# Optimization experiments

Measured on AMD Instinct MI355X. Metric: run time of the kernel, lower is better.

## Reference

```python
import jax, jax.numpy as jnp
import numpy as np

N_HEADS, N_KV_HEADS, HEAD_DIM = 32, 8, 128
N_REP = N_HEADS // N_KV_HEADS


def apply_rope(x, cos, sin):
    # x: [B, H, T, D]; cos/sin: [T, D/2]. Interleaved complex rotation (LLaMA style).
    x1 = x[..., 0::2]
    x2 = x[..., 1::2]
    c = cos[None, None, :, :]
    s = sin[None, None, :, :]
    r1 = x1 * c - x2 * s
    r2 = x1 * s + x2 * c
    return jnp.stack([r1, r2], axis=-1).reshape(x.shape)


def setup_inputs() -> dict:
    key = jax.random.key(0)
    ks = jax.random.split(key, 7)
    B, T, D = 1, 2048, 4096
    sc = 0.02
    return {
        "x": jax.random.normal(ks[0], (B, T, D), jnp.float32),
        "cos": jnp.cos(jax.random.normal(ks[1], (T, HEAD_DIM // 2), jnp.float32)),
        "sin": jnp.sin(jax.random.normal(ks[1], (T, HEAD_DIM // 2), jnp.float32)),
        "wq": jax.random.normal(ks[2], (D, D), jnp.float32) * sc,
        "wk": jax.random.normal(ks[3], (N_KV_HEADS * HEAD_DIM, D), jnp.float32) * sc,
        "wv": jax.random.normal(ks[4], (N_KV_HEADS * HEAD_DIM, D), jnp.float32) * sc,
        "wo": jax.random.normal(ks[5], (D, D), jnp.float32) * sc,
    }


def reference(x, cos, sin, wq, wk, wv, wo):
    B, T, _ = x.shape
    # QKV projections (nn.Linear: y = x @ W^T)
    q = (x @ wq.T).reshape(B, T, N_HEADS, HEAD_DIM).transpose(0, 2, 1, 3)
    k = (x @ wk.T).reshape(B, T, N_KV_HEADS, HEAD_DIM).transpose(0, 2, 1, 3)
    v = (x @ wv.T).reshape(B, T, N_KV_HEADS, HEAD_DIM).transpose(0, 2, 1, 3)
    # RoPE on q, k
    q = apply_rope(q, cos[:T], sin[:T])
    k = apply_rope(k, cos[:T], sin[:T])
    # GQA: repeat_interleave kv heads along head dim
    if N_REP > 1:
        k = jnp.repeat(k, N_REP, axis=1)
        v = jnp.repeat(v, N_REP, axis=1)
    # causal SDPA
    scale = 1.0 / jnp.sqrt(jnp.float32(HEAD_DIM))
    scores = jnp.einsum("bhqd,bhkd->bhqk", q, k) * scale
    causal = jnp.tril(jnp.ones((T, T), dtype=bool))
    scores = jnp.where(causal[None, None], scores, jnp.finfo(scores.dtype).min)
    attn = jax.nn.softmax(scores, axis=-1)
    y = jnp.einsum("bhqk,bhkd->bhqd", attn, v)
    y = y.transpose(0, 2, 1, 3).reshape(B, T, -1)
    return y @ wo.T
```

## Files before the change

### kernel.cpp

```cpp
#include <hip/hip_runtime.h>
#include <stdint.h>

typedef unsigned short ushort_t;
typedef __attribute__((ext_vector_type(8))) __bf16 bf16x8;
typedef __attribute__((ext_vector_type(4))) float f32x4;
typedef __attribute__((ext_vector_type(16))) float f32x16;

#define MFMA16(a, b, c) __builtin_amdgcn_mfma_f32_16x16x32_bf16((a), (b), (c), 0, 0, 0)
#define MFMA32(a, b, c) __builtin_amdgcn_mfma_f32_32x32x16_bf16((a), (b), (c), 0, 0, 0)

__device__ __forceinline__ ushort_t f2bf(float f) {
    unsigned u = __float_as_uint(f);
    u += 0x7fffu + ((u >> 16) & 1u);
    return (ushort_t)(u >> 16);
}

typedef __attribute__((address_space(1))) const unsigned char g_u8;
typedef __attribute__((address_space(3))) unsigned char l_u8;
__device__ __forceinline__ void gload16(const void* g, void* l) {
    __builtin_amdgcn_global_load_lds((g_u8*)g, (l_u8*)(unsigned int)(uintptr_t)l, 16, 0, 0);
}

__global__ __launch_bounds__(256) void cast_multi(const float* __restrict__ x,
                                                  const float* __restrict__ wq,
                                                  const float* __restrict__ wk,
                                                  const float* __restrict__ wv,
                                                  ushort_t* __restrict__ xb,
                                                  ushort_t* __restrict__ wqb,
                                                  ushort_t* __restrict__ wkb,
                                                  ushort_t* __restrict__ wvb) {
    int i = blockIdx.x * 256 + threadIdx.x;
    const float* in; ushort_t* out; int off;
    if (i < 2097152)      { in = x;  out = xb;  off = i; }
    else if (i < 6291456) { in = wq; out = wqb; off = i - 2097152; }
    else if (i < 7340032) { in = wk; out = wkb; off = i - 6291456; }
    else                  { in = wv; out = wvb; off = i - 7340032; }
    float4 v = ((const float4*)in)[off];
    ushort4 o;
    o.x = f2bf(v.x); o.y = f2bf(v.y); o.z = f2bf(v.z); o.w = f2bf(v.w);
    ((ushort4*)out)[off] = o;
}

__global__ __launch_bounds__(256) void cast_f32_bf16(const float* __restrict__ in,
                                                     ushort_t* __restrict__ out, int n4) {
    int i = blockIdx.x * 256 + threadIdx.x;
    if (i < n4) {
        float4 v = ((const float4*)in)[i];
        ushort4 o;
        o.x = f2bf(v.x); o.y = f2bf(v.y); o.z = f2bf(v.z); o.w = f2bf(v.w);
        ((ushort4*)out)[i] = o;
    }
}

#define GEMM_K_LOOP(Aarr, Barr, KDIM)                                                   \
    const ushort_t* aptr[4]; const ushort_t* bptr[4]; int ldsoff[4];                    \
    _Pragma("unroll")                                                                   \
    for (int p = 0; p < 4; p++) {                                                       \
        int s = p * 256 + tid;                                                          \
        int row = s >> 3;                                                               \
        int kc = (s & 7) ^ (row & 7);                                                   \
        aptr[p] = Aarr + (size_t)(bm + row) * (KDIM) + kc * 8;                          \
        bptr[p] = Barr + (size_t)(bn + row) * (KDIM) + kc * 8;                          \
        ldsoff[p] = s * 8;                                                              \
    }                                                                                   \
    const int l32 = lane & 31, hi = lane >> 5, r7 = l32 & 7;                            \
    for (int k0 = 0; k0 < (KDIM); k0 += 64) {                                           \
        _Pragma("unroll")                                                               \
        for (int p = 0; p < 4; p++) {                                                   \
            gload16(aptr[p] + k0, As + ldsoff[p]);                                      \
            gload16(bptr[p] + k0, Bs + ldsoff[p]);                                      \
        }                                                                               \
        __syncthreads();                                                                \
        _Pragma("unroll")                                                               \
        for (int ks = 0; ks < 4; ks++) {                                                \
            const int swz = ((ks * 2 + hi) ^ r7) << 3;                                  \
            bf16x8 a0 = *(const bf16x8*)(&As[(wm + l32) * 64 + swz]);                   \
            bf16x8 a1 = *(const bf16x8*)(&As[(wm + 32 + l32) * 64 + swz]);              \
            bf16x8 b0 = *(const bf16x8*)(&Bs[(wn + l32) * 64 + swz]);                   \
            bf16x8 b1 = *(const bf16x8*)(&Bs[(wn + 32 + l32) * 64 + swz]);              \
            acc[0][0] = MFMA32(a0, b0, acc[0][0]);                                      \
            acc[0][1] = MFMA32(a0, b1, acc[0][1]);                                      \
            acc[1][0] = MFMA32(a1, b0, acc[1][0]);                                      \
            acc[1][1] = MFMA32(a1, b1, acc[1][1]);                                      \
        }                                                                               \
        __syncthreads();                                                                \
    }

__global__ __launch_bounds__(256, 3) void gemm_qkv(const ushort_t* __restrict__ A,
                                                   const ushort_t* __restrict__ Wq,
                                                   const ushort_t* __restrict__ Wk,
                                                   const ushort_t* __restrict__ Wv,
                                                   ushort_t* __restrict__ Qo,
                                                   ushort_t* __restrict__ Ko,
                                                   ushort_t* __restrict__ VtO,
                                                   const float* __restrict__ cosp,
                                                   const float* __restrict__ sinp,
                                                   const float* __restrict__ wo,
                                                   ushort_t* __restrict__ wob) {
    const int by = blockIdx.y;
    const int tid = threadIdx.x;

    if (by >= 48) {
        const int ci = (by - 48) * gridDim.x + blockIdx.x;
        const float4* src = (const float4*)wo;
        ushort4* dst = (ushort4*)wob;
        int base = ci * 4096 + tid;
#pragma unroll
        for (int p = 0; p < 16; p++) {
            float4 v = src[base + p * 256];
            ushort4 o;
            o.x = f2bf(v.x); o.y = f2bf(v.y); o.z = f2bf(v.z); o.w = f2bf(v.w);
            dst[base + p * 256] = o;
        }
        return;
    }

    const ushort_t* B;
    int region, bn;
    if (by < 32)      { region = 0; B = Wq; bn = by * 128; }
    else if (by < 40) { region = 1; B = Wk; bn = (by - 32) * 128; }
    else              { region = 2; B = Wv; bn = (by - 40) * 128; }
    const int bm = blockIdx.x * 128;

    __shared__ __align__(16) ushort_t As[128 * 64];
    __shared__ __align__(16) ushort_t Bs[128 * 64];
    const int w = tid >> 6, lane = tid & 63;
    const int wm = (w >> 1) * 64, wn = (w & 1) * 64;
    f32x16 acc[2][2] = {};

    GEMM_K_LOOP(A, B, 4096)

    const float qscale = 0.08838834764831845f;
    if (region < 2) {
        ushort_t* C = (region == 0) ? Qo : Ko;
        const int Nc = (region == 0) ? 4096 : 1024;
        const float scl = (region == 0) ? qscale : 1.0f;
#pragma unroll
        for (int i = 0; i < 2; i++)
#pragma unroll
            for (int j = 0; j < 2; j++) {
                const int col = bn + wn + j * 32 + l32;
                const int pj = (col & 127) >> 1;
#pragma unroll
                for (int r = 0; r < 16; r++) {
                    const int row = bm + wm + i * 32 + (r & 3) + 8 * (r >> 2) + 4 * hi;
                    float v = acc[i][j][r];
                    float p = __shfl_xor(v, 1);
                    float c = cosp[row * 64 + pj], s = sinp[row * 64 + pj];
                    float res = (col & 1) ? fmaf(p, s, v * c)
                                          : (v * c - p * s);
                    C[(size_t)row * Nc + col] = f2bf(res * scl);
                }
            }
    } else {
#pragma unroll
        for (int i = 0; i < 2; i++)
#pragma unroll
            for (int j = 0; j < 2; j++) {
                const int col = bn + wn + j * 32 + l32;
#pragma unroll
                for (int g = 0; g < 4; g++) {
                    const int rowb = bm + wm + i * 32 + g * 8 + 4 * hi;
                    ushort4 pk;
                    pk.x = f2bf(acc[i][j][g * 4 + 0]);
                    pk.y = f2bf(acc[i][j][g * 4 + 1]);
                    pk.z = f2bf(acc[i][j][g * 4 + 2]);
                    pk.w = f2bf(acc[i][j][g * 4 + 3]);
                    *(ushort4*)(VtO + (size_t)col * 2048 + rowb) = pk;
                }
            }
    }
}

__global__ __launch_bounds__(256, 3) void gemm_bt(const ushort_t* __restrict__ A,
                                                  const ushort_t* __restrict__ B,
                                                  float* __restrict__ C,
                                                  int M, int N, int K) {
    const int bm = blockIdx.x * 128, bn = blockIdx.y * 128;
    __shared__ __align__(16) ushort_t As[128 * 64];
    __shared__ __align__(16) ushort_t Bs[128 * 64];
    const int tid = threadIdx.x;
    const int w = tid >> 6, lane = tid & 63;
    const int wm = (w >> 1) * 64, wn = (w & 1) * 64;
    f32x16 acc[2][2] = {};

    GEMM_K_LOOP(A, B, K)

#pragma unroll
    for (int i = 0; i < 2; i++)
#pragma unroll
        for (int j = 0; j < 2; j++) {
            const int col = bn + wn + j * 32 + l32;
#pragma unroll
            for (int r = 0; r < 16; r++) {
                const int row = bm + wm + i * 32 + (r & 3) + 8 * (r >> 2) + 4 * hi;
                C[(size_t)row * N + col] = acc[i][j][r];
            }
        }
}

__global__ __launch_bounds__(256) void flash_attn(const ushort_t* __restrict__ Q,
                                                  const ushort_t* __restrict__ Kp,
                                                  const ushort_t* __restrict__ Vt,
                                                  ushort_t* __restrict__ Y) {
    const int h = blockIdx.y, kh = h >> 2;
    const int tid = threadIdx.x;
    const int w = tid >> 6, lane = tid & 63;
    const int quad = lane >> 4, l16 = lane & 15;

    __shared__ __align__(16) ushort_t Ks[64 * 136];
    __shared__ __align__(16) ushort_t VtS[128 * 88];
    __shared__ __align__(16) ushort_t Ps[4 * 16 * 88];

    bf16x8 ones;
#pragma unroll
    for (int e = 0; e < 8; e++) ((ushort_t*)&ones)[e] = 0x3F80;

#pragma unroll 1
    for (int phase = 0; phase < 2; phase++) {
        const int qt = (phase == 0) ? blockIdx.x : 31 - blockIdx.x;

        bf16x8 qf[4];
        {
            const ushort_t* qrow = Q + (size_t)(qt * 64 + w * 16 + l16) * 4096 + h * 128 + quad * 8;
#pragma unroll
            for (int ks = 0; ks < 4; ks++) qf[ks] = *(const bf16x8*)(qrow + ks * 32);
        }

        f32x4 o[8] = {};
        f32x4 lacc = {};
        float m_i[4];
#pragma unroll
        for (int r = 0; r < 4; r++) m_i[r] = -1e30f;

        const int ntiles = qt + 1;
        for (int j = 0; j < ntiles; j++) {
            const int t0 = j * 64;
            {
#pragma unroll
                for (int p = 0; p < 4; p++) {
                    int ck = p * 256 + tid;
                    int r = ck >> 4, c = (ck & 15) * 8;
                    uint4 d = *(const uint4*)(Kp + (size_t)(t0 + r) * 1024 + kh * 128 + c);
                    *(uint4*)(&Ks[r * 136 + c]) = d;
                }
            }
            {
#pragma unroll
                for (int p = 0; p < 4; p++) {
                    int ck = p * 256 + tid;
                    int d = ck >> 3, c = (ck & 7) * 8;
                    uint4 v = *(const uint4*)(Vt + (size_t)(kh * 128 + d) * 2048 + t0 + c);
                    *(uint4*)(&VtS[d * 88 + c]) = v;
                }
            }
            __syncthreads();

            f32x4 s[4] = {};
#pragma unroll
            for (int ct = 0; ct < 4; ct++)
#pragma unroll
                for (int ks = 0; ks < 4; ks++) {
                    bf16x8 kf = *(const bf16x8*)(&Ks[(ct * 16 + l16) * 136 + ks * 32 + quad * 8]);
                    s[ct] = MFMA16(qf[ks], kf, s[ct]);
                }

            if (j == qt) {
#pragma unroll
                for (int ct = 0; ct < 4; ct++)
#pragma unroll
                    for (int r = 0; r < 4; r++) {
                        int rg = w * 16 + quad * 4 + r;
                        int cg = ct * 16 + l16;
                        if (cg > rg) s[ct][r] = -1e30f;
                    }
            }

            float alpha[4];
#pragma unroll
            for (int r = 0; r < 4; r++) {
                float v = fmaxf(fmaxf(s[0][r], s[1][r]), fmaxf(s[2][r], s[3][r]));
                v = fmaxf(v, __shfl_xor(v, 1));
                v = fmaxf(v, __shfl_xor(v, 2));
                v = fmaxf(v, __shfl_xor(v, 4));
                v = fmaxf(v, __shfl_xor(v, 8));
                float mn = fmaxf(m_i[r], v);
                alpha[r] = __expf(m_i[r] - mn);
                m_i[r] = mn;
            }
#pragma unroll
            for (int ct = 0; ct < 4; ct++)
#pragma unroll
                for (int r = 0; r < 4; r++)
                    s[ct][r] = __expf(s[ct][r] - m_i[r]);
#pragma unroll
            for (int n = 0; n < 8; n++)
#pragma unroll
                for (int r = 0; r < 4; r++) o[n][r] *= alpha[r];
#pragma unroll
            for (int r = 0; r < 4; r++) lacc[r] *= alpha[r];

#pragma unroll
            for (int ct = 0; ct < 4; ct++)
#pragma unroll
                for (int r = 0; r < 4; r++)
                    Ps[w * 1408 + (quad * 4 + r) * 88 + ct * 16 + l16] = f2bf(s[ct][r]);
            __threadfence_block();

#pragma unroll
            for (int ks2 = 0; ks2 < 2; ks2++) {
                bf16x8 pf = *(const bf16x8*)(&Ps[w * 1408 + l16 * 88 + ks2 * 32 + quad * 8]);
                lacc = MFMA16(pf, ones, lacc);
#pragma unroll
                for (int n = 0; n < 8; n++) {
                    bf16x8 vf = *(const bf16x8*)(&VtS[(n * 16 + l16) * 88 + ks2 * 32 + quad * 8]);
                    o[n] = MFMA16(pf, vf, o[n]);
                }
            }
            __syncthreads();
        }

        float inv[4];
#pragma unroll
        for (int r = 0; r < 4; r++) inv[r] = 1.0f / lacc[r];
#pragma unroll
        for (int n = 0; n < 8; n++)
#pragma unroll
            for (int r = 0; r < 4; r++) {
                int row = qt * 64 + w * 16 + quad * 4 + r;
                int col = h * 128 + n * 16 + l16;
                Y[(size_t)row * 4096 + col] = f2bf(o[n][r] * inv[r]);
            }
    }
}

extern "C" void kernel_launch(void* const* d_in, const int* in_sizes, int n_in,
                              void* d_out, int out_size, void* d_ws, size_t ws_size,
                              hipStream_t stream) {
    const float* x    = (const float*)d_in[0];
    const float* cosp = (const float*)d_in[1];
    const float* sinp = (const float*)d_in[2];
    const float* wq   = (const float*)d_in[3];
    const float* wk   = (const float*)d_in[4];
    const float* wv   = (const float*)d_in[5];
    const float* wo   = (const float*)d_in[6];
    float* out = (float*)d_out;

    ushort_t* xb   = (ushort_t*)d_ws;
    ushort_t* qb   = xb  + (size_t)2048 * 4096;
    ushort_t* yb   = qb  + (size_t)2048 * 4096;
    ushort_t* kb   = yb  + (size_t)2048 * 4096;
    ushort_t* vtb  = kb  + (size_t)2048 * 1024;
    ushort_t* wkb  = vtb + (size_t)1024 * 2048;
    ushort_t* wvb  = wkb + (size_t)1024 * 4096;
    ushort_t* wbig = wvb + (size_t)1024 * 4096;
    ushort_t* wob  = wbig + (size_t)4096 * 4096;
    const size_t need_fused = (size_t)(wob + (size_t)4096 * 4096 - xb) * sizeof(ushort_t);
    const bool fuse_wo = ws_size >= need_fused;

    cast_multi<<<32768, 256, 0, stream>>>(x, wq, wk, wv, xb, wbig, wkb, wvb);

    {
        dim3 g(16, fuse_wo ? 112 : 48, 1);
        gemm_qkv<<<g, 256, 0, stream>>>(xb, wbig, wkb, wvb, qb, kb, vtb, cosp, sinp,
                                        wo, fuse_wo ? wob : wbig);
    }

    {
        dim3 g(16, 32, 1);
        flash_attn<<<g, 256, 0, stream>>>(qb, kb, vtb, yb);
    }

    const ushort_t* wo_b = fuse_wo ? wob : wbig;
    if (!fuse_wo)
        cast_f32_bf16<<<16384, 256, 0, stream>>>(wo, wbig, 4096 * 4096 / 4);
    {
        dim3 g(16, 32, 1);
        gemm_bt<<<g, 256, 0, stream>>>(yb, wo_b, out, 2048, 4096, 4096);
    }
}
```

Baseline: 478.3 us.

## Enlarge GEMM tiles to 512-thread blocks with multi-buffered LDS prefetch pipeline

Replaces the single-buffered GEMM K-loop with a software-pipelined loop. A tiles are double-buffered and B tiles triple-buffered in LDS. Next-tile global-to-LDS loads are interleaved across the MFMA sub-steps, with explicit vmcnt waits, barriers and setprio. The QKV GEMM moves to 256x256 tiles with 512 threads, and the output GEMM to 256x128 tiles. The grids and the fused wo-cast indexing are rebuilt to match. This aims to hide global load latency and raise data reuse per tile. The cost is fewer blocks than CUs for the QKV GEMM and LDS use near the per-CU limit.

```diff
diff --git a/kernel.cpp b/kernel.cpp
--- a/kernel.cpp
+++ b/kernel.cpp
@@ -8,6 +8,9 @@
 
 #define MFMA16(a, b, c) __builtin_amdgcn_mfma_f32_16x16x32_bf16((a), (b), (c), 0, 0, 0)
 #define MFMA32(a, b, c) __builtin_amdgcn_mfma_f32_32x32x16_bf16((a), (b), (c), 0, 0, 0)
+
+#define STR_(x) #x
+#define STR(x) STR_(x)
 
 __device__ __forceinline__ ushort_t f2bf(float f) {
     unsigned u = __float_as_uint(f);
@@ -52,41 +55,93 @@
     }
 }
 
-#define GEMM_K_LOOP(Aarr, Barr, KDIM)                                                   \
-    const ushort_t* aptr[4]; const ushort_t* bptr[4]; int ldsoff[4];                    \
-    _Pragma("unroll")                                                                   \
-    for (int p = 0; p < 4; p++) {                                                       \
-        int s = p * 256 + tid;                                                          \
-        int row = s >> 3;                                                               \
-        int kc = (s & 7) ^ (row & 7);                                                   \
-        aptr[p] = Aarr + (size_t)(bm + row) * (KDIM) + kc * 8;                          \
-        bptr[p] = Barr + (size_t)(bn + row) * (KDIM) + kc * 8;                          \
-        ldsoff[p] = s * 8;                                                              \
-    }                                                                                   \
-    const int l32 = lane & 31, hi = lane >> 5, r7 = l32 & 7;                            \
-    for (int k0 = 0; k0 < (KDIM); k0 += 64) {                                           \
-        _Pragma("unroll")                                                               \
-        for (int p = 0; p < 4; p++) {                                                   \
-            gload16(aptr[p] + k0, As + ldsoff[p]);                                      \
-            gload16(bptr[p] + k0, Bs + ldsoff[p]);                                      \
-        }                                                                               \
-        __syncthreads();                                                                \
-        _Pragma("unroll")                                                               \
-        for (int ks = 0; ks < 4; ks++) {                                                \
-            const int swz = ((ks * 2 + hi) ^ r7) << 3;                                  \
-            bf16x8 a0 = *(const bf16x8*)(&As[(wm + l32) * 64 + swz]);                   \
-            bf16x8 a1 = *(const bf16x8*)(&As[(wm + 32 + l32) * 64 + swz]);              \
-            bf16x8 b0 = *(const bf16x8*)(&Bs[(wn + l32) * 64 + swz]);                   \
-            bf16x8 b1 = *(const bf16x8*)(&Bs[(wn + 32 + l32) * 64 + swz]);              \
-            acc[0][0] = MFMA32(a0, b0, acc[0][0]);                                      \
-            acc[0][1] = MFMA32(a0, b1, acc[0][1]);                                      \
-            acc[1][0] = MFMA32(a1, b0, acc[1][0]);                                      \
-            acc[1][1] = MFMA32(a1, b1, acc[1][1]);                                      \
-        }                                                                               \
-        __syncthreads();                                                                \
-    }
-
-__global__ __launch_bounds__(256, 3) void gemm_qkv(const ushort_t* __restrict__ A,
+#define GEMM_K_LOOP_8P(Aarr, Barr, KDIM, AI, BJ, ALOADS, BLOADS, VM)                     \
+    const int l32 = lane & 31, hi = lane >> 5, r7 = l32 & 7;                             \
+    const int srow = tid >> 3;                                                           \
+    const int skc = (tid & 7) ^ (srow & 7);                                              \
+    const ushort_t* aS = (Aarr) + (size_t)(bm + srow) * (KDIM) + skc * 8;                \
+    const ushort_t* bS = (Barr) + (size_t)(bn + srow) * (KDIM) + skc * 8;                \
+    const int lofs = tid * 8;                                                            \
+    const int NT = (KDIM) >> 6;                                                          \
+    _Pragma("unroll")                                                                    \
+    for (int p = 0; p < (ALOADS); p++)                                                   \
+        gload16(aS + (size_t)p * 64 * (KDIM), &Asl[0][lofs + p * 4096]);                 \
+    _Pragma("unroll")                                                                    \
+    for (int p = 0; p < (BLOADS); p++)                                                   \
+        gload16(bS + (size_t)p * 64 * (KDIM), &Bsl[0][lofs + p * 4096]);                 \
+    _Pragma("unroll")                                                                    \
+    for (int p = 0; p < (BLOADS); p++)                                                   \
+        gload16(bS + (size_t)p * 64 * (KDIM) + 64, &Bsl[1][lofs + p * 4096]);            \
+    asm volatile("s_waitcnt vmcnt(" STR(VM) ")" ::: "memory");                           \
+    __builtin_amdgcn_s_barrier();                                                        \
+    asm volatile("" ::: "memory");                                                       \
+    int cbB = 0, sbB = 2;                                                                \
+    for (int t = 0; t < NT; t++) {                                                       \
+        const int cbA = t & 1;                                                           \
+        const ushort_t* Ab = Asl[cbA];                                                   \
+        const ushort_t* Bb = Bsl[cbB];                                                   \
+        ushort_t* AbS = Asl[cbA ^ 1];                                                    \
+        ushort_t* BbS = Bsl[sbB];                                                        \
+        const bool stA = (t + 1 < NT);                                                   \
+        const bool stB = (t + 2 < NT);                                                   \
+        const size_t koA = (size_t)(t + 1) * 64;                                         \
+        const size_t koB = (size_t)(t + 2) * 64;                                         \
+        _Pragma("unroll")                                                                \
+        for (int ks = 0; ks < 4; ks++) {                                                 \
+            const int swz = ((ks * 2 + hi) ^ r7) << 3;                                   \
+            bf16x8 af[AI], bfr[BJ];                                                      \
+            _Pragma("unroll")                                                            \
+            for (int i = 0; i < (AI); i++)                                               \
+                af[i] = *(const bf16x8*)(&Ab[(wm + i * 32 + l32) * 64 + swz]);           \
+            _Pragma("unroll")                                                            \
+            for (int j = 0; j < (BJ); j++)                                               \
+                bfr[j] = *(const bf16x8*)(&Bb[(wn + j * 32 + l32) * 64 + swz]);          \
+            if (ks == 0 && stA) {                                                        \
+                _Pragma("unroll")                                                        \
+                for (int p = 0; p < (ALOADS) / 2; p++)                                   \
+                    gload16(aS + koA + (size_t)p * 64 * (KDIM), &AbS[lofs + p * 4096]);  \
+            }                                                                            \
+            if (ks == 1 && stA) {                                                        \
+                _Pragma("unroll")                                                        \
+                for (int p = (ALOADS) / 2; p < (ALOADS); p++)                            \
+                    gload16(aS + koA + (size_t)p * 64 * (KDIM), &AbS[lofs + p * 4096]);  \
+            }                                                                            \
+            if (ks == 2 && stB) {                                                        \
+                _Pragma("unroll")                                                        \
+                for (int p = 0; p < (BLOADS) / 2; p++)                                   \
+                    gload16(bS + koB + (size_t)p * 64 * (KDIM), &BbS[lofs + p * 4096]);  \
+            }                                                                            \
+            if (ks == 3 && stB) {                                                        \
+                _Pragma("unroll")                                                        \
+                for (int p = (BLOADS) / 2; p < (BLOADS); p++)                            \
+                    gload16(bS + koB + (size_t)p * 64 * (KDIM), &BbS[lofs + p * 4096]);  \
+            }                                                                            \
+            __builtin_amdgcn_s_barrier();                                                \
+            asm volatile("s_waitcnt lgkmcnt(0)" ::: "memory");                           \
+            __builtin_amdgcn_sched_barrier(0);                                           \
+            __builtin_amdgcn_s_setprio(1);                                               \
+            _Pragma("unroll")                                                            \
+            for (int i = 0; i < (AI); i++) {                                             \
+                _Pragma("unroll")                                                        \
+                for (int j = 0; j < (BJ); j++)                                           \
+                    acc[i][j] = MFMA32(af[i], bfr[j], acc[i][j]);                        \
+            }                                                                            \
+            __builtin_amdgcn_s_setprio(0);                                               \
+            if (ks < 3) {                                                                \
+                __builtin_amdgcn_s_barrier();                                            \
+            } else {                                                                     \
+                if (stB) { asm volatile("s_waitcnt vmcnt(" STR(VM) ")" ::: "memory"); }  \
+                else     { asm volatile("s_waitcnt vmcnt(0)" ::: "memory"); }            \
+                __builtin_amdgcn_s_barrier();                                            \
+                asm volatile("" ::: "memory");                                           \
+                __builtin_amdgcn_sched_barrier(0);                                       \
+            }                                                                            \
+        }                                                                                \
+        if (++cbB == 3) cbB = 0;                                                         \
+        if (++sbB == 3) sbB = 0;                                                         \
+    }
+
+__global__ __launch_bounds__(512, 2) void gemm_qkv(const ushort_t* __restrict__ A,
                                                    const ushort_t* __restrict__ Wq,
                                                    const ushort_t* __restrict__ Wk,
                                                    const ushort_t* __restrict__ Wv,
@@ -100,35 +155,35 @@
     const int by = blockIdx.y;
     const int tid = threadIdx.x;
 
-    if (by >= 48) {
-        const int ci = (by - 48) * gridDim.x + blockIdx.x;
+    if (by >= 24) {
+        const int ci = (by - 24) * gridDim.x + blockIdx.x;
         const float4* src = (const float4*)wo;
         ushort4* dst = (ushort4*)wob;
-        int base = ci * 4096 + tid;
+        int base = ci * 8192 + tid;
 #pragma unroll
         for (int p = 0; p < 16; p++) {
-            float4 v = src[base + p * 256];
+            float4 v = src[base + p * 512];
             ushort4 o;
             o.x = f2bf(v.x); o.y = f2bf(v.y); o.z = f2bf(v.z); o.w = f2bf(v.w);
-            dst[base + p * 256] = o;
+            dst[base + p * 512] = o;
         }
         return;
     }
 
     const ushort_t* B;
     int region, bn;
-    if (by < 32)      { region = 0; B = Wq; bn = by * 128; }
-    else if (by < 40) { region = 1; B = Wk; bn = (by - 32) * 128; }
-    else              { region = 2; B = Wv; bn = (by - 40) * 128; }
-    const int bm = blockIdx.x * 128;
-
-    __shared__ __align__(16) ushort_t As[128 * 64];
-    __shared__ __align__(16) ushort_t Bs[128 * 64];
+    if (by < 16)      { region = 0; B = Wq; bn = by * 256; }
+    else if (by < 20) { region = 1; B = Wk; bn = (by - 16) * 256; }
+    else              { region = 2; B = Wv; bn = (by - 20) * 256; }
+    const int bm = blockIdx.x * 256;
+
+    __shared__ __align__(16) ushort_t Asl[2][256 * 64];
+    __shared__ __align__(16) ushort_t Bsl[3][256 * 64];
     const int w = tid >> 6, lane = tid & 63;
-    const int wm = (w >> 1) * 64, wn = (w & 1) * 64;
-    f32x16 acc[2][2] = {};
-
-    GEMM_K_LOOP(A, B, 4096)
+    const int wm = (w >> 2) * 128, wn = (w & 3) * 64;
+    f32x16 acc[4][2] = {};
+
+    GEMM_K_LOOP_8P(A, B, 4096, 4, 2, 4, 4, 4)
 
     const float qscale = 0.08838834764831845f;
     if (region < 2) {
@@ -136,7 +191,7 @@
         const int Nc = (region == 0) ? 4096 : 1024;
         const float scl = (region == 0) ? qscale : 1.0f;
 #pragma unroll
-        for (int i = 0; i < 2; i++)
+        for (int i = 0; i < 4; i++)
 #pragma unroll
             for (int j = 0; j < 2; j++) {
                 const int col = bn + wn + j * 32 + l32;
@@ -154,7 +209,7 @@
             }
     } else {
 #pragma unroll
-        for (int i = 0; i < 2; i++)
+        for (int i = 0; i < 4; i++)
 #pragma unroll
             for (int j = 0; j < 2; j++) {
                 const int col = bn + wn + j * 32 + l32;
@@ -172,19 +227,19 @@
     }
 }
 
-__global__ __launch_bounds__(256, 3) void gemm_bt(const ushort_t* __restrict__ A,
+__global__ __launch_bounds__(512, 2) void gemm_bt(const ushort_t* __restrict__ A,
                                                   const ushort_t* __restrict__ B,
                                                   float* __restrict__ C,
                                                   int M, int N, int K) {
-    const int bm = blockIdx.x * 128, bn = blockIdx.y * 128;
-    __shared__ __align__(16) ushort_t As[128 * 64];
-    __shared__ __align__(16) ushort_t Bs[128 * 64];
+    const int bm = blockIdx.x * 256, bn = blockIdx.y * 128;
+    __shared__ __align__(16) ushort_t Asl[2][256 * 64];
+    __shared__ __align__(16) ushort_t Bsl[3][128 * 64];
     const int tid = threadIdx.x;
     const int w = tid >> 6, lane = tid & 63;
     const int wm = (w >> 1) * 64, wn = (w & 1) * 64;
     f32x16 acc[2][2] = {};
 
-    GEMM_K_LOOP(A, B, K)
+    GEMM_K_LOOP_8P(A, B, K, 2, 2, 4, 2, 2)
 
 #pragma unroll
     for (int i = 0; i < 2; i++)
@@ -361,8 +416,8 @@
     cast_multi<<<32768, 256, 0, stream>>>(x, wq, wk, wv, xb, wbig, wkb, wvb);
 
     {
-        dim3 g(16, fuse_wo ? 112 : 48, 1);
-        gemm_qkv<<<g, 256, 0, stream>>>(xb, wbig, wkb, wvb, qb, kb, vtb, cosp, sinp,
+        dim3 g(8, fuse_wo ? 88 : 24, 1);
+        gemm_qkv<<<g, 512, 0, stream>>>(xb, wbig, wkb, wvb, qb, kb, vtb, cosp, sinp,
                                         wo, fuse_wo ? wob : wbig);
     }
 
@@ -375,7 +430,7 @@
     if (!fuse_wo)
         cast_f32_bf16<<<16384, 256, 0, stream>>>(wo, wbig, 4096 * 4096 / 4);
     {
-        dim3 g(16, 32, 1);
-        gemm_bt<<<g, 256, 0, stream>>>(yb, wo_b, out, 2048, 4096, 4096);
-    }
-}
+        dim3 g(8, 32, 1);
+        gemm_bt<<<g, 512, 0, stream>>>(yb, wo_b, out, 2048, 4096, 4096);
+    }
+}
```

Result: faster. 467.0 us (-2.4%).

## Triple-buffer output-projection GEMM with 256x128 tiles and 512 threads

Applied to the files above, without the earlier changes.

Rewrites the output-projection GEMM to use 512-thread blocks computing 256x128 tiles, with a three-stage LDS ring buffer fed by direct global-to-LDS loads. Loads for tile t+2 are spread across the four k-substeps and interleaved with MFMA issue, using wave priority raising and explicit waitcnt and barrier placement. The goal is to hide global load latency and improve operand reuse. In exchange it uses more LDS per block (about 144 KB), halves the grid to 256 blocks, and adds a barrier at every k-substep.

```diff
diff --git a/kernel.cpp b/kernel.cpp
--- a/kernel.cpp
+++ b/kernel.cpp
@@ -172,19 +172,87 @@
     }
 }
 
-__global__ __launch_bounds__(256, 3) void gemm_bt(const ushort_t* __restrict__ A,
+__global__ __launch_bounds__(512, 2) void gemm_bt(const ushort_t* __restrict__ A,
                                                   const ushort_t* __restrict__ B,
                                                   float* __restrict__ C,
                                                   int M, int N, int K) {
-    const int bm = blockIdx.x * 128, bn = blockIdx.y * 128;
-    __shared__ __align__(16) ushort_t As[128 * 64];
-    __shared__ __align__(16) ushort_t Bs[128 * 64];
+    const int bm = blockIdx.x * 256, bn = blockIdx.y * 128;
+    __shared__ __align__(16) ushort_t Asl[3][256 * 64];
+    __shared__ __align__(16) ushort_t Bsl[3][128 * 64];
     const int tid = threadIdx.x;
     const int w = tid >> 6, lane = tid & 63;
     const int wm = (w >> 1) * 64, wn = (w & 1) * 64;
     f32x16 acc[2][2] = {};
 
-    GEMM_K_LOOP(A, B, K)
+    const int l32 = lane & 31, hi = lane >> 5, r7 = l32 & 7;
+    const int srow = tid >> 3;
+    const int skc = (tid & 7) ^ (srow & 7);
+    const ushort_t* aS = A + (size_t)(bm + srow) * K + skc * 8;
+    const ushort_t* bS = B + (size_t)(bn + srow) * K + skc * 8;
+    const int lofs = tid * 8;
+    const int NT = K >> 6;
+
+#pragma unroll
+    for (int p = 0; p < 4; p++) gload16(aS + (size_t)p * 64 * K, &Asl[0][lofs + p * 4096]);
+#pragma unroll
+    for (int p = 0; p < 2; p++) gload16(bS + (size_t)p * 64 * K, &Bsl[0][lofs + p * 4096]);
+#pragma unroll
+    for (int p = 0; p < 4; p++) gload16(aS + 64 + (size_t)p * 64 * K, &Asl[1][lofs + p * 4096]);
+#pragma unroll
+    for (int p = 0; p < 2; p++) gload16(bS + 64 + (size_t)p * 64 * K, &Bsl[1][lofs + p * 4096]);
+    asm volatile("s_waitcnt vmcnt(6)" ::: "memory");
+    __builtin_amdgcn_s_barrier();
+    asm volatile("" ::: "memory");
+
+    int cb = 0, sb = 2;
+    for (int t = 0; t < NT; t++) {
+        const ushort_t* Ab = Asl[cb];
+        const ushort_t* Bb = Bsl[cb];
+        ushort_t* AbS = Asl[sb];
+        ushort_t* BbS = Bsl[sb];
+        const bool st = (t + 2 < NT);
+        const size_t ko = (size_t)(t + 2) * 64;
+#pragma unroll
+        for (int ks = 0; ks < 4; ks++) {
+            const int swz = ((ks * 2 + hi) ^ r7) << 3;
+            bf16x8 a0 = *(const bf16x8*)(&Ab[(wm + l32) * 64 + swz]);
+            bf16x8 a1 = *(const bf16x8*)(&Ab[(wm + 32 + l32) * 64 + swz]);
+            bf16x8 b0 = *(const bf16x8*)(&Bb[(wn + l32) * 64 + swz]);
+            bf16x8 b1 = *(const bf16x8*)(&Bb[(wn + 32 + l32) * 64 + swz]);
+            if (st) {
+                if (ks == 0) {
+                    gload16(aS + ko, &AbS[lofs]);
+                    gload16(aS + ko + (size_t)64 * K, &AbS[lofs + 4096]);
+                }
+                if (ks == 1) {
+                    gload16(aS + ko + (size_t)128 * K, &AbS[lofs + 8192]);
+                    gload16(aS + ko + (size_t)192 * K, &AbS[lofs + 12288]);
+                }
+                if (ks == 2) gload16(bS + ko, &BbS[lofs]);
+                if (ks == 3) gload16(bS + ko + (size_t)64 * K, &BbS[lofs + 4096]);
+            }
+            __builtin_amdgcn_s_barrier();
+            asm volatile("s_waitcnt lgkmcnt(0)" ::: "memory");
+            __builtin_amdgcn_sched_barrier(0);
+            __builtin_amdgcn_s_setprio(1);
+            acc[0][0] = MFMA32(a0, b0, acc[0][0]);
+            acc[0][1] = MFMA32(a0, b1, acc[0][1]);
+            acc[1][0] = MFMA32(a1, b0, acc[1][0]);
+            acc[1][1] = MFMA32(a1, b1, acc[1][1]);
+            __builtin_amdgcn_s_setprio(0);
+            if (ks < 3) {
+                __builtin_amdgcn_s_barrier();
+            } else {
+                if (st) { asm volatile("s_waitcnt vmcnt(6)" ::: "memory"); }
+                else    { asm volatile("s_waitcnt vmcnt(0)" ::: "memory"); }
+                __builtin_amdgcn_s_barrier();
+                asm volatile("" ::: "memory");
+                __builtin_amdgcn_sched_barrier(0);
+            }
+        }
+        if (++cb == 3) cb = 0;
+        if (++sb == 3) sb = 0;
+    }
 
 #pragma unroll
     for (int i = 0; i < 2; i++)
@@ -375,7 +443,7 @@
     if (!fuse_wo)
         cast_f32_bf16<<<16384, 256, 0, stream>>>(wo, wbig, 4096 * 4096 / 4);
     {
-        dim3 g(16, 32, 1);
-        gemm_bt<<<g, 256, 0, stream>>>(yb, wo_b, out, 2048, 4096, 4096);
-    }
-}
+        dim3 g(8, 32, 1);
+        gemm_bt<<<g, 512, 0, stream>>>(yb, wo_b, out, 2048, 4096, 4096);
+    }
+}
```

Result: no change. 474.0 us (-0.9%).
